# Optimization experiments

Hardware: AMD Instinct MI355X
Metric: run time of the kernel (lower is better)

Reference implementation:

```python
import jax, jax.numpy as jnp
import numpy as np

N_NODES = 100000
N_EDGES = 1600000
PERIODS = 12
HIDDEN = 32  # hard-coded out_channels in the module


def setup_inputs() -> dict:
    key = jax.random.key(0)
    ks = jax.random.split(key, 16)
    inp = {
        "x": jax.random.normal(ks[0], (N_NODES, PERIODS), jnp.float32),
        "edge_index": jax.random.randint(ks[1], (2, N_EDGES), 0, N_NODES, jnp.int64),
        "edge_weight": jax.random.uniform(ks[2], (N_EDGES,), jnp.float32),
        # A3TGCN attention over periods
        "attention": jax.random.normal(ks[3], (PERIODS,), jnp.float32),
        # TGCN cell params: GCNConv(1 -> 32) and Linear(64 -> 32) per gate (z, r, h)
        "conv_z_w": jax.random.normal(ks[4], (1, HIDDEN), jnp.float32) * 0.5,
        "conv_z_b": jnp.zeros((HIDDEN,), jnp.float32),
        "lin_z_w": jax.random.normal(ks[5], (2 * HIDDEN, HIDDEN), jnp.float32) * 0.1,
        "lin_z_b": jnp.zeros((HIDDEN,), jnp.float32),
        "conv_r_w": jax.random.normal(ks[6], (1, HIDDEN), jnp.float32) * 0.5,
        "conv_r_b": jnp.zeros((HIDDEN,), jnp.float32),
        "lin_r_w": jax.random.normal(ks[7], (2 * HIDDEN, HIDDEN), jnp.float32) * 0.1,
        "lin_r_b": jnp.zeros((HIDDEN,), jnp.float32),
        "conv_h_w": jax.random.normal(ks[8], (1, HIDDEN), jnp.float32) * 0.5,
        "conv_h_b": jnp.zeros((HIDDEN,), jnp.float32),
        "lin_h_w": jax.random.normal(ks[9], (2 * HIDDEN, HIDDEN), jnp.float32) * 0.1,
        "lin_h_b": jnp.zeros((HIDDEN,), jnp.float32),
        # head Linear(32 -> 1)
        "head_w": jax.random.normal(ks[10], (HIDDEN, 1), jnp.float32) * 0.1,
        "head_b": jnp.zeros((1,), jnp.float32),
    }
    return inp


def reference(x, edge_index, edge_weight, attention,
              conv_z_w, conv_z_b, lin_z_w, lin_z_b,
              conv_r_w, conv_r_b, lin_r_w, lin_r_b,
              conv_h_w, conv_h_b, lin_h_w, lin_h_b,
              head_w, head_b):
    N, T = x.shape
    src, dst = edge_index[0], edge_index[1]
    # GCN normalization with self loops (fill value 1.0)
    loop = jnp.arange(N)
    src_f = jnp.concatenate([src, loop])
    dst_f = jnp.concatenate([dst, loop])
    ew_f = jnp.concatenate([edge_weight, jnp.ones((N,), x.dtype)])
    deg = jax.ops.segment_sum(ew_f, dst_f, num_segments=N)
    dinv = jnp.where(deg > 0, deg, 1.0) ** -0.5
    norm = dinv[src_f] * ew_f * dinv[dst_f]
    # propagate raw features for ALL periods at once (in_channels=1, so
    # A_hat @ (x W) == (A_hat @ x) W; propagate-then-transform is cheaper).
    agg = jax.ops.segment_sum(norm[:, None] * x[src_f], dst_f, num_segments=N)  # [N, T]

    def conv(w, b):  # GCNConv(1->32) applied to every period -> [N, T, 32]
        return agg[..., None] * w[0] + b

    Cz, Cr, Ch = conv(conv_z_w, conv_z_b), conv(conv_r_w, conv_r_b), conv(conv_h_w, conv_h_b)
    # A3TGCN passes H=None to every period's TGCN cell -> H = 0
    H = jnp.zeros_like(Cz)
    Z = jax.nn.sigmoid(jnp.concatenate([Cz, H], -1) @ lin_z_w + lin_z_b)
    R = jax.nn.sigmoid(jnp.concatenate([Cr, H], -1) @ lin_r_w + lin_r_b)
    Ht = jnp.tanh(jnp.concatenate([Ch, H * R], -1) @ lin_h_w + lin_h_b)
    Hc = Z * H + (1.0 - Z) * Ht  # [N, T, 32]
    probs = jax.nn.softmax(attention)  # attention over periods
    H_accum = jnp.einsum('t,nto->no', probs, Hc)  # [N, 32]
    h = jax.nn.relu(H_accum)
    return h @ head_w + head_b  # [N, 1]
```

## Files before the change

kernel.cpp:

```cpp
#include <hip/hip_runtime.h>

#define NN 100000
#define NE 1600000
#define TT 12
#define HH 32
#define NB 391
#define NCH 391
#define BSH 8
#define CHUNK 4096
#define SORTCAP 4800
#define LOG2E 1.4426950408889634f

typedef unsigned int u32;


__global__ __launch_bounds__(512) void k_scatter(const int* __restrict__ ei,
                                                 const float* __restrict__ ew,
                                                 int2* __restrict__ rec,
                                                 int* __restrict__ offT,
                                                 const float* __restrict__ czw, const float* __restrict__ czb,
                                                 const float* __restrict__ lzw, const float* __restrict__ lzb,
                                                 const float* __restrict__ chw, const float* __restrict__ chb,
                                                 const float* __restrict__ lhw, const float* __restrict__ lhb,
                                                 const float* __restrict__ att, float* __restrict__ P) {
    int t = threadIdx.x;
    if (blockIdx.x == NCH) {
        if (t < HH) {
            int j = t;
            float az = 0.f, bz = 0.f, ah = 0.f, bh = 0.f;
            for (int k = 0; k < HH; ++k) {
                float lz = lzw[k * HH + j];
                float lh = lhw[k * HH + j];
                az = fmaf(czw[k], lz, az);
                bz = fmaf(czb[k], lz, bz);
                ah = fmaf(chw[k], lh, ah);
                bh = fmaf(chb[k], lh, bh);
            }
            P[j]        = az * LOG2E;
            P[HH + j]   = (bz + lzb[j]) * LOG2E;
            P[2*HH + j] = 2.0f * LOG2E * ah;
            P[3*HH + j] = 2.0f * LOG2E * (bh + lhb[j]);
        }
        if (t == 0) {
            float m = -1e30f;
            for (int q = 0; q < TT; ++q) m = fmaxf(m, att[q]);
            float ex[TT]; float s = 0.f;
            for (int q = 0; q < TT; ++q) { ex[q] = expf(att[q] - m); s += ex[q]; }
            for (int q = 0; q < TT; ++q) P[4*HH + q] = ex[q] / s;
        }
        return;
    }
    __shared__ int2 cbuf[CHUNK];
    __shared__ int sc[512];
    __shared__ int cnt[NB], off[NB], cur[NB];
    int base = blockIdx.x * CHUNK;
    int m = min(CHUNK, NE - base);
    for (int j = t; j < NB; j += 512) { cnt[j] = 0; cur[j] = 0; }
    __syncthreads();
    int dsts[8], srcs[8]; float ews[8];
#pragma unroll
    for (int i = 0; i < 8; ++i) {
        int k = t + i * 512;
        if (k < m) {
            int e = base + k;
            dsts[i] = ei[NE + e]; srcs[i] = ei[e]; ews[i] = ew[e];
            atomicAdd(&cnt[dsts[i] >> BSH], 1);
        }
    }
    __syncthreads();
    int v = (t < NB) ? cnt[t] : 0;
    sc[t] = v;
    __syncthreads();
    for (int o = 1; o < 512; o <<= 1) {
        int add = (t >= o) ? sc[t - o] : 0;
        __syncthreads();
        sc[t] += add;
        __syncthreads();
    }
    if (t < NB) {
        int e = sc[t] - v;
        off[t] = e;
        offT[blockIdx.x * 392 + t] = e;
    }
    if (t == 0) offT[blockIdx.x * 392 + NB] = m;
    __syncthreads();
#pragma unroll
    for (int i = 0; i < 8; ++i) {
        int k = t + i * 512;
        if (k < m) {
            int b = dsts[i] >> BSH;
            int p = off[b] + atomicAdd(&cur[b], 1);
            cbuf[p] = make_int2(srcs[i] | ((dsts[i] & 255) << 17), __float_as_int(ews[i]));
        }
    }
    __syncthreads();
    for (int k = t; k < m; k += 512) rec[base + k] = cbuf[k];
}

__device__ __forceinline__ u32 bfpack(float a, float b) {
    u32 ua = __float_as_uint(a), ub = __float_as_uint(b);
    ua = (ua + 0x7FFFu + ((ua >> 16) & 1u)) >> 16;
    ub = (ub + 0x7FFFu + ((ub >> 16) & 1u)) >> 16;
    return ua | (ub << 16);
}

__global__ __launch_bounds__(512) void k_sort(const int2* __restrict__ rec,
                                              const int* __restrict__ offT,
                                              int2* __restrict__ rec2,
                                              int* __restrict__ nodebase,
                                              int* __restrict__ bend,
                                              float* __restrict__ dinv,
                                              const float* __restrict__ x,
                                              u32* __restrict__ xpb) {
    __shared__ int2 buf[SORTCAP];
    __shared__ int sc[512];
    __shared__ int cnt[256], cur[256];
    __shared__ float wsum[256], dvs[256];
    int b = blockIdx.x, t = threadIdx.x;
    int o0 = 0, len = 0;
    if (t < NCH) {
        o0 = offT[t * 392 + b];
        len = offT[t * 392 + b + 1] - o0;
    }
    sc[t] = len;
    __syncthreads();
    for (int o = 1; o < 512; o <<= 1) {
        int add = (t >= o) ? sc[t - o] : 0;
        __syncthreads();
        sc[t] += add;
        __syncthreads();
    }
    int rdst = sc[t] - len;
    int m = min(sc[511], SORTCAP);
    if (t < 256) { cnt[t] = 0; wsum[t] = 0.f; }
    __syncthreads();
    for (int j = 0; j < len; ++j) {
        int d = rdst + j;
        if (d >= SORTCAP) break;
        int2 r = rec[t * CHUNK + o0 + j];
        buf[d] = r;
        int loc = (r.x >> 17) & 255;
        atomicAdd(&cnt[loc], 1);
        atomicAdd(&wsum[loc], __int_as_float(r.y));
    }
    __syncthreads();
    int v = (t < 256) ? cnt[t] : 0;
    sc[t] = v;
    __syncthreads();
    for (int o = 1; o < 256; o <<= 1) {
        int add = (t >= o) ? sc[t - o] : 0;
        __syncthreads();
        sc[t] += add;
        __syncthreads();
    }
    if (t < 256) {
        int e = sc[t] - v;
        cur[t] = e;
        float dv = rsqrtf(1.0f + wsum[t]);
        dvs[t] = dv;
        int n = (b << BSH) + t;
        if (n < NN) {
            dinv[n] = dv;
            nodebase[n] = b * SORTCAP + e;
            const float4* xr = (const float4*)(x + (long)n * TT);
            float4 v0 = xr[0], v1 = xr[1], v2 = xr[2];
            uint4* xo = (uint4*)(xpb + ((long)n << 3));
            uint4 w0, w1;
            w0.x = bfpack(v0.x * dv, v0.y * dv);
            w0.y = bfpack(v0.z * dv, v0.w * dv);
            w0.z = bfpack(v1.x * dv, v1.y * dv);
            w0.w = bfpack(v1.z * dv, v1.w * dv);
            w1.x = bfpack(v2.x * dv, v2.y * dv);
            w1.y = bfpack(v2.z * dv, v2.w * dv);
            w1.z = 0u; w1.w = 0u;
            xo[0] = w0; xo[1] = w1;
        }
    }
    if (t == 0) {
        bend[b] = b * SORTCAP + m;
        if (b == NB - 1) nodebase[NN] = b * SORTCAP + m;
    }
    __syncthreads();
    for (int k = t; k < m; k += 512) {
        int2 r = buf[k];
        int loc = (r.x >> 17) & 255;
        int p = atomicAdd(&cur[loc], 1);
        float w2 = __int_as_float(r.y) * dvs[loc];
        rec2[b * SORTCAP + p] = make_int2(r.x & 0x1FFFF, __float_as_int(w2));
    }
}

#define BLO(w) __uint_as_float((w) << 16)
#define BHI(w) __uint_as_float((w) & 0xFFFF0000u)

__global__ __launch_bounds__(512) void k_fused(const int* __restrict__ nodebase,
                                               const int* __restrict__ bend,
                                               const int2* __restrict__ rec2,
                                               const float* __restrict__ dinv,
                                               const u32* __restrict__ xpb,
                                               const float* __restrict__ P,
                                               const float* __restrict__ hw,
                                               const float* __restrict__ hb,
                                               float* __restrict__ out) {
    int g = blockIdx.x * 512 + threadIdx.x;
    int n = g >> 4, sub = g & 15;
    float a[TT];
#pragma unroll
    for (int q = 0; q < TT; ++q) a[q] = 0.f;
    if (sub == 0) {
        float di = dinv[n];
        const uint4* xr = (const uint4*)(xpb + ((long)n << 3));
        uint4 h0 = xr[0];
        uint2 h1 = *(const uint2*)(xr + 1);
        a[0]  = di * BLO(h0.x); a[1]  = di * BHI(h0.x);
        a[2]  = di * BLO(h0.y); a[3]  = di * BHI(h0.y);
        a[4]  = di * BLO(h0.z); a[5]  = di * BHI(h0.z);
        a[6]  = di * BLO(h0.w); a[7]  = di * BHI(h0.w);
        a[8]  = di * BLO(h1.x); a[9]  = di * BHI(h1.x);
        a[10] = di * BLO(h1.y); a[11] = di * BHI(h1.y);
    }
    int k0 = nodebase[n];
    int k1 = ((n & 255) == 255) ? bend[n >> 8] : nodebase[n + 1];
    for (int k = k0 + sub; k < k1; k += 16) {
        int2 r = rec2[k];
        float c = __int_as_float(r.y);
        const uint4* xs = (const uint4*)(xpb + ((long)r.x << 3));
        uint4 h0 = xs[0];
        uint2 h1 = *(const uint2*)(xs + 1);
        a[0]  = fmaf(c, BLO(h0.x), a[0]);  a[1]  = fmaf(c, BHI(h0.x), a[1]);
        a[2]  = fmaf(c, BLO(h0.y), a[2]);  a[3]  = fmaf(c, BHI(h0.y), a[3]);
        a[4]  = fmaf(c, BLO(h0.z), a[4]);  a[5]  = fmaf(c, BHI(h0.z), a[5]);
        a[6]  = fmaf(c, BLO(h0.w), a[6]);  a[7]  = fmaf(c, BHI(h0.w), a[7]);
        a[8]  = fmaf(c, BLO(h1.x), a[8]);  a[9]  = fmaf(c, BHI(h1.x), a[9]);
        a[10] = fmaf(c, BLO(h1.y), a[10]); a[11] = fmaf(c, BHI(h1.y), a[11]);
    }
#pragma unroll
    for (int q = 0; q < TT; ++q) {
        float v = a[q];
        v += __shfl_xor(v, 1);
        v += __shfl_xor(v, 2);
        v += __shfl_xor(v, 4);
        v += __shfl_xor(v, 8);
        a[q] = v;
    }
    float p[TT];
#pragma unroll
    for (int q = 0; q < TT; ++q) p[q] = P[4*HH + q];
    float o = 0.f;
#pragma unroll
    for (int jj = 0; jj < 2; ++jj) {
        int j = (jj << 4) | sub;
        float Az = P[j], Bz = P[HH + j], Ah2 = P[2*HH + j], Bh2 = P[3*HH + j];
        float w = hw[j];
        float acc = 0.f;
#pragma unroll
        for (int q = 0; q < TT; ++q) {
            float xz = fmaf(a[q], Az, Bz);
            float xh = fminf(fmaf(a[q], Ah2, Bh2), 115.f);
            float ez = __builtin_amdgcn_exp2f(xz);
            float eh = __builtin_amdgcn_exp2f(xh);
            float den = (1.f + ez) * (eh + 1.f);
            float num = eh - 1.f;
            acc = fmaf(p[q] * num, __builtin_amdgcn_rcpf(den), acc);
        }
        o = fmaf(fmaxf(acc, 0.f), w, o);
    }
    o += __shfl_xor(o, 1);
    o += __shfl_xor(o, 2);
    o += __shfl_xor(o, 4);
    o += __shfl_xor(o, 8);
    if (sub == 0) out[n] = o + hb[0];
}

extern "C" void kernel_launch(void* const* d_in, const int* in_sizes, int n_in,
                              void* d_out, int out_size, void* d_ws, size_t ws_size,
                              hipStream_t stream) {
    const float* x    = (const float*)d_in[0];
    const int*   ei   = (const int*)d_in[1];
    const float* ew   = (const float*)d_in[2];
    const float* att  = (const float*)d_in[3];
    const float* czw  = (const float*)d_in[4];
    const float* czb  = (const float*)d_in[5];
    const float* lzw  = (const float*)d_in[6];
    const float* lzb  = (const float*)d_in[7];
    const float* chw  = (const float*)d_in[12];
    const float* chb  = (const float*)d_in[13];
    const float* lhw  = (const float*)d_in[14];
    const float* lhb  = (const float*)d_in[15];
    const float* hw   = (const float*)d_in[16];
    const float* hb   = (const float*)d_in[17];
    float* out = (float*)d_out;

    int*  ws32     = (int*)d_ws;
    int*  offT     = ws32;
    int*  nodebase = ws32 + 153280;
    int*  bend     = ws32 + 253312;
    float* dinv    = (float*)(ws32 + 253712);
    u32*  xpb      = (u32*)(ws32 + 353712);
    int2* rec      = (int2*)(ws32 + 1153712);
    int2* rec2     = (int2*)(ws32 + 4353712);
    float* P       = (float*)(ws32 + 8107312);

    k_scatter<<<NCH + 1, 512, 0, stream>>>(ei, ew, rec, offT,
                                           czw, czb, lzw, lzb, chw, chb, lhw, lhb, att, P);
    k_sort<<<NB, 512, 0, stream>>>(rec, offT, rec2, nodebase, bend, dinv, x, xpb);
    k_fused<<<(NN * 16) / 512, 512, 0, stream>>>(nodebase, bend, rec2, dinv, xpb,
                                                 P, hw, hb, out);
}
```

Baseline: 71.32 us.

## Shrink sort buckets to 64 nodes and rebalance scatter chunks across 512 blocks

Dest-node buckets shrink from 256 to 64 nodes, giving 1563 sort blocks instead of 391. Scatter now uses 512 chunks of 3125 edges, and each thread scans four bucket counts so the prefix sum still fits in 512 threads. The intent is more parallelism and better GPU occupancy in the sort stage, with smaller per-block LDS buffers. In exchange, the offset table grows and the sort kernel reads many more tiny segments per block, and the smaller SORTCAP raises the risk of overflowing a bucket when degrees are skewed.

```diff
diff --git a/kernel.cpp b/kernel.cpp
--- a/kernel.cpp
+++ b/kernel.cpp
@@ -4,11 +4,12 @@
 #define NE 1600000
 #define TT 12
 #define HH 32
-#define NB 391
-#define NCH 391
-#define BSH 8
-#define CHUNK 4096
-#define SORTCAP 4800
+#define NB 1563
+#define NBP 1564
+#define NCH 512
+#define BSH 6
+#define CHUNK 3125
+#define SORTCAP 1376
 #define LOG2E 1.4426950408889634f
 
 typedef unsigned int u32;
@@ -52,14 +53,14 @@
     }
     __shared__ int2 cbuf[CHUNK];
     __shared__ int sc[512];
-    __shared__ int cnt[NB], off[NB], cur[NB];
+    __shared__ int cnt[NBP], off[NBP], cur[NB];
     int base = blockIdx.x * CHUNK;
     int m = min(CHUNK, NE - base);
-    for (int j = t; j < NB; j += 512) { cnt[j] = 0; cur[j] = 0; }
-    __syncthreads();
-    int dsts[8], srcs[8]; float ews[8];
-#pragma unroll
-    for (int i = 0; i < 8; ++i) {
+    for (int j = t; j < NBP; j += 512) { cnt[j] = 0; if (j < NB) cur[j] = 0; }
+    __syncthreads();
+    int dsts[7], srcs[7]; float ews[7];
+#pragma unroll
+    for (int i = 0; i < 7; ++i) {
         int k = t + i * 512;
         if (k < m) {
             int e = base + k;
@@ -68,8 +69,13 @@
         }
     }
     __syncthreads();
-    int v = (t < NB) ? cnt[t] : 0;
-    sc[t] = v;
+    int j0 = 4 * t;
+    int c4[4]; int s = 0;
+    if (t < 391) {
+#pragma unroll
+        for (int i = 0; i < 4; ++i) { c4[i] = cnt[j0 + i]; s += c4[i]; }
+    }
+    sc[t] = (t < 391) ? s : 0;
     __syncthreads();
     for (int o = 1; o < 512; o <<= 1) {
         int add = (t >= o) ? sc[t - o] : 0;
@@ -77,20 +83,24 @@
         sc[t] += add;
         __syncthreads();
     }
-    if (t < NB) {
-        int e = sc[t] - v;
-        off[t] = e;
-        offT[blockIdx.x * 392 + t] = e;
-    }
-    if (t == 0) offT[blockIdx.x * 392 + NB] = m;
-    __syncthreads();
-#pragma unroll
-    for (int i = 0; i < 8; ++i) {
+    if (t < 391) {
+        int e = sc[t] - s;
+        int rowbase = blockIdx.x * NBP;
+#pragma unroll
+        for (int i = 0; i < 4; ++i) {
+            off[j0 + i] = e;
+            offT[rowbase + j0 + i] = e;
+            e += c4[i];
+        }
+    }
+    __syncthreads();
+#pragma unroll
+    for (int i = 0; i < 7; ++i) {
         int k = t + i * 512;
         if (k < m) {
             int b = dsts[i] >> BSH;
             int p = off[b] + atomicAdd(&cur[b], 1);
-            cbuf[p] = make_int2(srcs[i] | ((dsts[i] & 255) << 17), __float_as_int(ews[i]));
+            cbuf[p] = make_int2(srcs[i] | ((dsts[i] & 63) << 17), __float_as_int(ews[i]));
         }
     }
     __syncthreads();
@@ -114,15 +124,13 @@
                                               u32* __restrict__ xpb) {
     __shared__ int2 buf[SORTCAP];
     __shared__ int sc[512];
-    __shared__ int cnt[256], cur[256];
-    __shared__ float wsum[256], dvs[256];
+    __shared__ int cnt[64], cur[64];
+    __shared__ float wsum[64], dvs[64];
     int b = blockIdx.x, t = threadIdx.x;
-    int o0 = 0, len = 0;
-    if (t < NCH) {
-        o0 = offT[t * 392 + b];
-        len = offT[t * 392 + b + 1] - o0;
-    }
+    int o0 = offT[t * NBP + b];
+    int len = offT[t * NBP + b + 1] - o0;
     sc[t] = len;
+    if (t < 64) { cnt[t] = 0; wsum[t] = 0.f; }
     __syncthreads();
     for (int o = 1; o < 512; o <<= 1) {
         int add = (t >= o) ? sc[t - o] : 0;
@@ -132,28 +140,26 @@
     }
     int rdst = sc[t] - len;
     int m = min(sc[511], SORTCAP);
-    if (t < 256) { cnt[t] = 0; wsum[t] = 0.f; }
-    __syncthreads();
     for (int j = 0; j < len; ++j) {
         int d = rdst + j;
         if (d >= SORTCAP) break;
         int2 r = rec[t * CHUNK + o0 + j];
         buf[d] = r;
-        int loc = (r.x >> 17) & 255;
+        int loc = (r.x >> 17) & 63;
         atomicAdd(&cnt[loc], 1);
         atomicAdd(&wsum[loc], __int_as_float(r.y));
     }
     __syncthreads();
-    int v = (t < 256) ? cnt[t] : 0;
-    sc[t] = v;
-    __syncthreads();
-    for (int o = 1; o < 256; o <<= 1) {
-        int add = (t >= o) ? sc[t - o] : 0;
-        __syncthreads();
-        sc[t] += add;
-        __syncthreads();
-    }
-    if (t < 256) {
+    int v = (t < 64) ? cnt[t] : 0;
+    if (t < 64) sc[t] = v;
+    __syncthreads();
+    for (int o = 1; o < 64; o <<= 1) {
+        int add = (t < 64 && t >= o) ? sc[t - o] : 0;
+        __syncthreads();
+        if (t < 64) sc[t] += add;
+        __syncthreads();
+    }
+    if (t < 64) {
         int e = sc[t] - v;
         cur[t] = e;
         float dv = rsqrtf(1.0f + wsum[t]);
@@ -183,7 +189,7 @@
     __syncthreads();
     for (int k = t; k < m; k += 512) {
         int2 r = buf[k];
-        int loc = (r.x >> 17) & 255;
+        int loc = (r.x >> 17) & 63;
         int p = atomicAdd(&cur[loc], 1);
         float w2 = __int_as_float(r.y) * dvs[loc];
         rec2[b * SORTCAP + p] = make_int2(r.x & 0x1FFFF, __float_as_int(w2));
@@ -220,7 +226,7 @@
         a[10] = di * BLO(h1.y); a[11] = di * BHI(h1.y);
     }
     int k0 = nodebase[n];
-    int k1 = ((n & 255) == 255) ? bend[n >> 8] : nodebase[n + 1];
+    int k1 = ((n & 63) == 63) ? bend[n >> 6] : nodebase[n + 1];
     for (int k = k0 + sub; k < k1; k += 16) {
         int2 r = rec2[k];
         float c = __int_as_float(r.y);
@@ -293,13 +299,13 @@
 
     int*  ws32     = (int*)d_ws;
     int*  offT     = ws32;
-    int*  nodebase = ws32 + 153280;
-    int*  bend     = ws32 + 253312;
-    float* dinv    = (float*)(ws32 + 253712);
-    u32*  xpb      = (u32*)(ws32 + 353712);
-    int2* rec      = (int2*)(ws32 + 1153712);
-    int2* rec2     = (int2*)(ws32 + 4353712);
-    float* P       = (float*)(ws32 + 8107312);
+    int*  nodebase = ws32 + 800800;
+    int*  bend     = ws32 + 900816;
+    float* dinv    = (float*)(ws32 + 902400);
+    u32*  xpb      = (u32*)(ws32 + 1002400);
+    int2* rec      = (int2*)(ws32 + 1802400);
+    int2* rec2     = (int2*)(ws32 + 5002400);
+    float* P       = (float*)(ws32 + 9303776);
 
     k_scatter<<<NCH + 1, 512, 0, stream>>>(ei, ew, rec, offT,
                                            czw, czb, lzw, lzb, chw, chb, lhw, lhb, att, P);
```

New measurement: 76.17 us. +6.8%, slower.
